# Performance work log

Hardware: AMD Instinct MI355X
Metric: run time of the kernel (lower is better)

Reference implementation:

```python
import jax, jax.numpy as jnp
import numpy as np

CONFIGS = [(4, 2, 1, 1), (4, 4, 3, 3)]  # (k, stride, pad, dilation) per level


def conv2d(x, w, b, stride=1, pad=1):
    y = jax.lax.conv_general_dilated(x, w, (stride, stride), [(pad, pad), (pad, pad)],
                                     dimension_numbers=('NCHW', 'OIHW', 'NCHW'))
    return y + b[None, :, None, None]


def deform_conv(x, offset, mask, wgt, b, k, stride, pad, dil):
    """Modulated deformable conv v2 (zero padding, bilinear sampling).
    x: [B,Cin,Hin,Win]; offset: [B,2K,H,W] interleaved (dy_i,dx_i); mask: [B,K,H,W]."""
    B, Cin, Hin, Win = x.shape
    _, _, H, W = mask.shape
    K = k * k
    dy = offset[:, 0::2]  # [B,K,H,W]
    dx = offset[:, 1::2]
    ks = jnp.arange(k, dtype=offset.dtype) * dil
    kyf = jnp.repeat(ks, k)  # [K], ky-major to match weight.reshape(Cout,Cin,K)
    kxf = jnp.tile(ks, k)
    oy = jnp.arange(H, dtype=offset.dtype) * stride - pad
    ox = jnp.arange(W, dtype=offset.dtype) * stride - pad
    py = (kyf[:, None] + oy[None, :])[None, :, :, None] + dy  # [B,K,H,W]
    px = (kxf[:, None] + ox[None, :])[None, :, None, :] + dx

    def per_image(img, pyi, pxi, mi):
        imgf = img.reshape(Cin, -1)
        y0 = jnp.floor(pyi)
        x0 = jnp.floor(pxi)
        ly = pyi - y0
        lx = pxi - x0
        y0i = y0.astype(jnp.int32)
        x0i = x0.astype(jnp.int32)

        def corner(yi, xi, wt):
            valid = (yi >= 0) & (yi < Hin) & (xi >= 0) & (xi < Win)
            lin = (jnp.clip(yi, 0, Hin - 1) * Win + jnp.clip(xi, 0, Win - 1)).reshape(-1)
            v = imgf[:, lin].reshape(Cin, K, H, W)
            return v * (wt * valid)[None]

        s = (corner(y0i, x0i, (1 - ly) * (1 - lx))
             + corner(y0i, x0i + 1, (1 - ly) * lx)
             + corner(y0i + 1, x0i, ly * (1 - lx))
             + corner(y0i + 1, x0i + 1, ly * lx))
        return s * mi[None]  # [Cin,K,H,W]

    sampled = jax.vmap(per_image)(x, py, px, mask)  # [B,Cin,K,H,W]
    out = jnp.einsum('bikhw,oik->bohw', sampled, wgt.reshape(wgt.shape[0], Cin, K))
    return out + b[None, :, None, None]


def setup_inputs():
    key = jax.random.key(0)
    ks = jax.random.split(key, 16)
    B, C, H = 4, 256, 40
    K = 16  # k*k with k=4
    dcn_std = 1.0 / np.sqrt(C * K)
    res_std = 1.0 / np.sqrt(C * 9)
    return {
        'f0': jax.random.normal(ks[0], (B, C, H * 4, H * 4), jnp.float32),
        'f1': jax.random.normal(ks[1], (B, C, H * 2, H * 2), jnp.float32),
        'f2': jax.random.normal(ks[2], (B, C, H, H), jnp.float32),
        'com_w0': jax.random.normal(ks[3], (3 * K, C, 3, 3), jnp.float32) * 0.01,
        'com_b0': jax.random.normal(ks[4], (3 * K,), jnp.float32) * 0.01,
        'com_w1': jax.random.normal(ks[5], (3 * K, C, 3, 3), jnp.float32) * 0.01,
        'com_b1': jax.random.normal(ks[6], (3 * K,), jnp.float32) * 0.01,
        'dcn_w0': jax.random.normal(ks[7], (C, C, 4, 4), jnp.float32) * dcn_std,
        'dcn_b0': jnp.zeros((C,), jnp.float32),
        'dcn_w1': jax.random.normal(ks[8], (C, C, 4, 4), jnp.float32) * dcn_std,
        'dcn_b1': jnp.zeros((C,), jnp.float32),
        'res_w': jax.random.normal(ks[9], (C, C, 3, 3), jnp.float32) * res_std,
        'res_b': jnp.zeros((C,), jnp.float32),
    }


def reference(f0, f1, f2, com_w0, com_b0, com_w1, com_b1,
              dcn_w0, dcn_b0, dcn_w1, dcn_b1, res_w, res_b):
    features = [f0, f1, f2]
    com = [(com_w0, com_b0), (com_w1, com_b1)]
    dcn = [(dcn_w0, dcn_b0), (dcn_w1, dcn_b1)]
    repeat, levels = 2, 3
    fh = features[-1]
    f = fh
    for _ in range(repeat):
        for l in range(levels - 1):
            k, s, p, d = CONFIGS[l]
            K = k * k
            om = conv2d(f, com[l][0], com[l][1])
            offset = jnp.concatenate([om[:, :K], om[:, K:2 * K]], axis=1)
            m = jax.nn.sigmoid(om[:, 2 * K:])
            dc = deform_conv(features[levels - 2 - l], offset, m, dcn[l][0], dcn[l][1], k, s, p, d)
            f = jax.nn.relu(dc) + f
    return fh + conv2d(f, res_w, res_b)
```

## Files before the change

### kernel.cpp

```cpp
#include <hip/hip_runtime.h>

#define HW40 1600
typedef unsigned short ushort_t;
typedef __attribute__((ext_vector_type(8))) short short8;
typedef __attribute__((ext_vector_type(4))) short short4v;
typedef __attribute__((ext_vector_type(4))) float f4v;

__device__ __forceinline__ float bu(ushort_t u) {
  union { unsigned i; float f; } x; x.i = ((unsigned)u) << 16; return x.f;
}
__device__ __forceinline__ ushort_t fb(float f) {
  union { float f; unsigned i; } x; x.f = f;
  unsigned r = x.i + 0x7FFFu + ((x.i >> 16) & 1u);
  return (ushort_t)(r >> 16);
}

#define GLD16(g, l)                                                            \
  __builtin_amdgcn_global_load_lds(                                            \
      (const __attribute__((address_space(1))) void*)(g),                      \
      (__attribute__((address_space(3))) void*)(l), 16, 0, 0)

#define PART_STRIDE 1638400

__global__ __launch_bounds__(256) void prep_all(
    const float* __restrict__ com_w0, const float* __restrict__ com_w1,
    const float* __restrict__ res_w, const float* __restrict__ dcn_w0,
    const float* __restrict__ dcn_w1, ushort_t* __restrict__ Acom0,
    ushort_t* __restrict__ Acom1, ushort_t* __restrict__ Ares,
    ushort_t* __restrict__ A0, ushort_t* __restrict__ A1,
    ushort_t* __restrict__ zp) {
  __shared__ float s[4096];
  const int g = blockIdx.x;
  const int t = threadIdx.x;
  if (g < 3456) {
    const float* src; ushort_t* dst; int Cout_src; int base;
    if (g < 576)       { src = com_w0; dst = Acom0; Cout_src = 48;  base = g; }
    else if (g < 1152) { src = com_w1; dst = Acom1; Cout_src = 48;  base = g - 576; }
    else               { src = res_w;  dst = Ares;  Cout_src = 256; base = g - 1152; }
    const int idx = base * 256 + t;
    const int co = idx / 2304;
    const int k  = idx - co * 2304;
    const int cin = k & 255, tap = k >> 8;
    dst[idx] = (co < Cout_src) ? fb(src[(size_t)co * 2304 + cin * 9 + tap]) : (ushort_t)0;
  } else if (g < 3968) {
    const int lg = g - 3456;
    const int co = lg & 255;
    const float* w = (lg < 256) ? dcn_w0 : dcn_w1;
    ushort_t* A = (lg < 256) ? A0 : A1;
    const float4* wp = (const float4*)(w + (size_t)co * 4096);
#pragma unroll
    for (int q = 0; q < 4; ++q) ((float4*)s)[t + q * 256] = wp[t + q * 256];
    __syncthreads();
    const int i = t >> 4, cb = (t & 15) * 16;
    ushort_t tmp[16];
#pragma unroll
    for (int j = 0; j < 16; ++j) tmp[j] = fb(s[(cb + j) * 16 + i]);
    ushort_t* op = A + (size_t)co * 4096 + t * 16;
    ((uint4*)op)[0] = ((uint4*)tmp)[0];
    ((uint4*)op)[1] = ((uint4*)tmp)[1];
  } else {
    zp[t] = 0;
  }
}

__global__ __launch_bounds__(256) void nhwc_all(const float* __restrict__ f2,
                                                const float* __restrict__ f1,
                                                const float* __restrict__ f0,
                                                ushort_t* __restrict__ ft40,
                                                ushort_t* __restrict__ f1t,
                                                ushort_t* __restrict__ f0t) {
  __shared__ __align__(16) ushort_t tile[32][264];
  const int gx = blockIdx.x;
  const float* x; ushort_t* xt; int HW, sblk;
  if (gx < 50)       { x = f2; xt = ft40; HW = 1600;  sblk = gx; }
  else if (gx < 250) { x = f1; xt = f1t;  HW = 6400;  sblk = gx - 50; }
  else               { x = f0; xt = f0t;  HW = 25600; sblk = gx - 250; }
  const int s0 = sblk * 32, b = blockIdx.z;
  const int t = threadIdx.x;
  const int sp4 = (t & 7) * 4;
  const int cbase = (t >> 3) * 4;
  const float* xb = x + (size_t)b * 256 * HW + s0 + sp4;
#pragma unroll
  for (int q = 0; q < 2; ++q) {
    const int cc = cbase + q * 128;
    const float4 v0 = *(const float4*)(xb + (size_t)(cc + 0) * HW);
    const float4 v1 = *(const float4*)(xb + (size_t)(cc + 1) * HW);
    const float4 v2 = *(const float4*)(xb + (size_t)(cc + 2) * HW);
    const float4 v3 = *(const float4*)(xb + (size_t)(cc + 3) * HW);
    ushort_t p0[4] = {fb(v0.x), fb(v1.x), fb(v2.x), fb(v3.x)};
    ushort_t p1[4] = {fb(v0.y), fb(v1.y), fb(v2.y), fb(v3.y)};
    ushort_t p2[4] = {fb(v0.z), fb(v1.z), fb(v2.z), fb(v3.z)};
    ushort_t p3[4] = {fb(v0.w), fb(v1.w), fb(v2.w), fb(v3.w)};
    *(short4v*)(&tile[sp4 + 0][cc]) = *(short4v*)p0;
    *(short4v*)(&tile[sp4 + 1][cc]) = *(short4v*)p1;
    *(short4v*)(&tile[sp4 + 2][cc]) = *(short4v*)p2;
    *(short4v*)(&tile[sp4 + 3][cc]) = *(short4v*)p3;
  }
  __syncthreads();
  const int c8 = (t & 31) * 8;
  const int spb = t >> 5;
  ushort_t* ob = xt + ((size_t)b * HW + s0) * 256;
#pragma unroll
  for (int q2 = 0; q2 < 4; ++q2) {
    const int sp = spb + q2 * 8;
    short8 v = *(const short8*)(&tile[sp][c8]);
    *(short8*)(ob + (size_t)sp * 256 + c8) = v;
  }
}

__global__ __launch_bounds__(256) void sample_kernel(
    const ushort_t* __restrict__ xt, const ushort_t* __restrict__ part,
    const float* __restrict__ cbias, ushort_t* __restrict__ colT,
    int Hin, int Win, int stride, int pad, int dil) {
  __shared__ int4  gL[128];
  __shared__ float4 gW[128];
  const int g = blockIdx.x;
  const int work = (g & 7) * 100 + (g >> 3);
  const int b = work / 200;
  const int px0 = (work - b * 200) * 8;
  const int t = threadIdx.x;
  const int HWin = Hin * Win;

  if (t < 128) {
    const int px_l = t & 7, i = t >> 3;
    const int p = px0 + px_l;
    const int n = b * 1600 + p;
    const int ph = p / 40, pw = p - (p / 40) * 40;
    float dy = cbias[2 * i], dx = cbias[2 * i + 1], mzr = cbias[32 + i];
#pragma unroll
    for (int kz = 0; kz < 8; ++kz) {
      const ushort_t* pp = part + (size_t)kz * PART_STRIDE + n;
      dy  += bu(pp[(size_t)(2 * i) * 6400]);
      dx  += bu(pp[(size_t)(2 * i + 1) * 6400]);
      mzr += bu(pp[(size_t)(32 + i) * 6400]);
    }
    float mz = 1.f / (1.f + expf(-mzr));
    float py = (float)(ph * stride - pad + (i >> 2) * dil) + dy;
    float px = (float)(pw * stride - pad + (i & 3) * dil) + dx;
    float y0f = floorf(py), x0f = floorf(px);
    float ly = py - y0f, lx = px - x0f;
    int y0 = (int)y0f, x0 = (int)x0f;
    int y1 = y0 + 1, x1 = x0 + 1;
    float hy = 1.f - ly, hx = 1.f - lx;
    float w00 = hy * hx * mz, w01 = hy * lx * mz;
    float w10 = ly * hx * mz, w11 = ly * lx * mz;
    if (y0 < 0 || y0 >= Hin) { w00 = 0.f; w01 = 0.f; }
    if (y1 < 0 || y1 >= Hin) { w10 = 0.f; w11 = 0.f; }
    if (x0 < 0 || x0 >= Win) { w00 = 0.f; w10 = 0.f; }
    if (x1 < 0 || x1 >= Win) { w01 = 0.f; w11 = 0.f; }
    int cy0 = min(max(y0, 0), Hin - 1), cy1 = min(max(y1, 0), Hin - 1);
    int cx0 = min(max(x0, 0), Win - 1), cx1 = min(max(x1, 0), Win - 1);
    gL[t] = make_int4((cy0 * Win + cx0) * 256, (cy0 * Win + cx1) * 256,
                      (cy1 * Win + cx0) * 256, (cy1 * Win + cx1) * 256);
    gW[t] = make_float4(w00, w01, w10, w11);
  }
  __syncthreads();

  const ushort_t* xtb = xt + (size_t)b * HWin * 256;
  const int wv = t >> 6, l = t & 63;
  const int half = l >> 5;
  const int cin8 = (l & 31) * 8;

#pragma unroll 2
  for (int it = 0; it < 16; ++it) {
    const int pr = it * 8 + wv * 2 + half;
    const int4 G = gL[pr];
    const float4 W = gW[pr];
    short8 c00 = *(const short8*)(xtb + G.x + cin8);
    short8 c01 = *(const short8*)(xtb + G.y + cin8);
    short8 c10 = *(const short8*)(xtb + G.z + cin8);
    short8 c11 = *(const short8*)(xtb + G.w + cin8);
    short8 rr;
#pragma unroll
    for (int j = 0; j < 8; ++j) {
      float v = W.x * bu((ushort_t)c00[j]) + W.y * bu((ushort_t)c01[j]) +
                W.z * bu((ushort_t)c10[j]) + W.w * bu((ushort_t)c11[j]);
      rr[j] = (short)fb(v);
    }
    const int px_l = pr & 7, i = pr >> 3;
    *(short8*)(colT + ((size_t)(b * 1600 + px0 + px_l) * 4096 + i * 256 + cin8)) = rr;
  }
}

__global__ __launch_bounds__(256) void gemm_deform(const ushort_t* __restrict__ A,
                                                   const ushort_t* __restrict__ B,
                                                   ushort_t* __restrict__ part) {
  __shared__ ushort_t sA[128 * 32];
  __shared__ ushort_t sB[128 * 32];
  const int g = blockIdx.x;
  const int kz = g & 3, mt = (g >> 2) & 1, nt = g >> 3;
  const int t = threadIdx.x;
  const int wv = t >> 6, l = t & 63;
  const int wm = wv >> 1, wn = wv & 1;

  f4v acc[4][4];
#pragma unroll
  for (int a = 0; a < 4; ++a)
#pragma unroll
    for (int bb = 0; bb < 4; ++bb) acc[a][bb] = (f4v)(0.f);

  const int ra = t >> 2;
  const int q  = ((t & 3) - (ra >> 1)) & 3;
  const size_t aoff = (size_t)(mt * 128 + ra) * 4096 + q * 8;
  const size_t boff = (size_t)(nt * 128 + ra) * 4096 + q * 8;
  ushort_t* lA = sA + t * 8;
  ushort_t* lB = sB + t * 8;

  int k0 = kz * 1024;
  const int lm = l & 15;
  const int koff = (((l >> 4) + (lm >> 1)) & 3) * 8;

  for (int step = 0; step < 32; ++step, k0 += 32) {
    __syncthreads();
    GLD16(A + aoff + k0, lA);
    GLD16(A + aoff + (size_t)64 * 4096 + k0, lA + 2048);
    GLD16(B + boff + k0, lB);
    GLD16(B + boff + (size_t)64 * 4096 + k0, lB + 2048);
    __syncthreads();
    short8 af[4], bfr[4];
#pragma unroll
    for (int fm = 0; fm < 4; ++fm)
      af[fm] = *(const short8*)(sA + (wm * 64 + fm * 16 + lm) * 32 + koff);
#pragma unroll
    for (int fn = 0; fn < 4; ++fn)
      bfr[fn] = *(const short8*)(sB + (wn * 64 + fn * 16 + lm) * 32 + koff);
#pragma unroll
    for (int fm = 0; fm < 4; ++fm)
#pragma unroll
      for (int fn = 0; fn < 4; ++fn)
        acc[fm][fn] = __builtin_amdgcn_mfma_f32_16x16x32_bf16(af[fm], bfr[fn],
                                                              acc[fm][fn], 0, 0, 0);
  }

  const int row_l = (l >> 4) * 4;
  ushort_t* pb = part + (size_t)kz * PART_STRIDE;
#pragma unroll
  for (int fm = 0; fm < 4; ++fm) {
#pragma unroll
    for (int fn = 0; fn < 4; ++fn) {
      const int n = nt * 128 + wn * 64 + fn * 16 + lm;
#pragma unroll
      for (int r = 0; r < 4; ++r) {
        const int m = mt * 128 + wm * 64 + fm * 16 + row_l + r;
        pb[(size_t)m * 6400 + n] = fb(acc[fm][fn][r]);
      }
    }
  }
}

template <int MTILE, int KZ>
__global__ __launch_bounds__(256) void gemm_conv3(const ushort_t* __restrict__ A,
                                                  const ushort_t* __restrict__ ft,
                                                  const ushort_t* __restrict__ zp,
                                                  ushort_t* __restrict__ part,
                                                  int ksteps) {
  constexpr int FN = (MTILE == 128) ? 4 : 2;
  __shared__ ushort_t sA[MTILE * 32];
  __shared__ ushort_t sB[128 * 32];
  const int g = blockIdx.x;
  const int kz = g % KZ;
  const int r = g / KZ;
  const int mt = (MTILE == 128) ? (r & 1) : 0;
  const int nt = (MTILE == 128) ? (r >> 1) : r;
  const int t = threadIdx.x;
  const int wv = t >> 6, l = t & 63;
  const int wm = (MTILE == 128) ? (wv >> 1) : 0;
  const int wn = (MTILE == 128) ? (wv & 1) : wv;

  f4v acc[4][FN];
#pragma unroll
  for (int a = 0; a < 4; ++a)
#pragma unroll
    for (int bb = 0; bb < FN; ++bb) acc[a][bb] = (f4v)(0.f);

  const int ra = t >> 2;
  const int q  = ((t & 3) - (ra >> 1)) & 3;
  const int qc = q * 8;
  const size_t aoff = (size_t)(mt * MTILE + ra) * 2304 + qc;
  const int n0 = nt * 128 + ra;
  const int n1 = n0 + 64;
  const int b0 = n0 / 1600, p0 = n0 - b0 * 1600;
  const int b1 = n1 / 1600, p1 = n1 - b1 * 1600;
  const int ph0 = p0 / 40, pw0 = p0 - (p0 / 40) * 40;
  const int ph1 = p1 / 40, pw1 = p1 - (p1 / 40) * 40;
  const ushort_t* fp0 = ft + (size_t)n0 * 256 + qc;
  const ushort_t* fp1 = ft + (size_t)n1 * 256 + qc;
  ushort_t* lA = sA + t * 8;
  ushort_t* lB = sB + t * 8;

  int k0 = kz * ksteps * 32;
  const int lm = l & 15;
  const int koff = (((l >> 4) + (lm >> 1)) & 3) * 8;

  for (int step = 0; step < ksteps; ++step, k0 += 32) {
    const int tap = k0 >> 8, c0 = k0 & 255;
    const int ky = tap / 3;
    const int dy = ky - 1, dx = (tap - ky * 3) - 1;
    const int off = (dy * 40 + dx) * 256 + c0;
    const bool ok0 = ((unsigned)(ph0 + dy) < 40u) & ((unsigned)(pw0 + dx) < 40u);
    const bool ok1 = ((unsigned)(ph1 + dy) < 40u) & ((unsigned)(pw1 + dx) < 40u);
    const ushort_t* s0 = ok0 ? (fp0 + off) : zp;
    const ushort_t* s1 = ok1 ? (fp1 + off) : zp;
    __syncthreads();
    GLD16(A + aoff + k0, lA);
    if (MTILE == 128) GLD16(A + aoff + (size_t)64 * 2304 + k0, lA + 2048);
    GLD16(s0, lB);
    GLD16(s1, lB + 2048);
    __syncthreads();
    short8 af[4], bfr[FN];
#pragma unroll
    for (int fm = 0; fm < 4; ++fm)
      af[fm] = *(const short8*)(sA + (wm * 64 + fm * 16 + lm) * 32 + koff);
#pragma unroll
    for (int fn = 0; fn < FN; ++fn)
      bfr[fn] = *(const short8*)(sB + (wn * (16 * FN) + fn * 16 + lm) * 32 + koff);
#pragma unroll
    for (int fm = 0; fm < 4; ++fm)
#pragma unroll
      for (int fn = 0; fn < FN; ++fn)
        acc[fm][fn] = __builtin_amdgcn_mfma_f32_16x16x32_bf16(af[fm], bfr[fn],
                                                              acc[fm][fn], 0, 0, 0);
  }

  const int row_l = (l >> 4) * 4;
  ushort_t* pb = part + (size_t)kz * PART_STRIDE;
#pragma unroll
  for (int fm = 0; fm < 4; ++fm) {
#pragma unroll
    for (int fn = 0; fn < FN; ++fn) {
      const int n = nt * 128 + wn * (16 * FN) + fn * 16 + lm;
#pragma unroll
      for (int r = 0; r < 4; ++r) {
        const int m = mt * MTILE + wm * 64 + fm * 16 + row_l + r;
        pb[(size_t)m * 6400 + n] = fb(acc[fm][fn][r]);
      }
    }
  }
}

template <int NKZ>
__global__ __launch_bounds__(256) void epi_fused(const ushort_t* __restrict__ part,
                                                 const float* __restrict__ bias,
                                                 const float* __restrict__ src,
                                                 float* __restrict__ dst,
                                                 ushort_t* __restrict__ ft, int relu) {
  __shared__ __align__(16) ushort_t tile[32][72];
  const int t = threadIdx.x;
  const int p0 = blockIdx.x * 64, c0 = blockIdx.y * 32, b = blockIdx.z;
  const int co_l = t >> 3, pg = t & 7;
  const int co = c0 + co_l;
  const size_t n = (size_t)b * 1600 + p0 + pg * 8;

  float a[8] = {0.f, 0.f, 0.f, 0.f, 0.f, 0.f, 0.f, 0.f};
#pragma unroll
  for (int kz = 0; kz < NKZ; ++kz) {
    short8 pp = *(const short8*)(part + (size_t)kz * PART_STRIDE + (size_t)co * 6400 + n);
#pragma unroll
    for (int j = 0; j < 8; ++j) a[j] += bu((ushort_t)pp[j]);
  }
  const float bv = bias[co];
  const size_t fo = ((size_t)b * 256 + co) * 1600 + p0 + pg * 8;
  float4 s0 = *(const float4*)(src + fo);
  float4 s1 = *(const float4*)(src + fo + 4);
  const float sv[8] = {s0.x, s0.y, s0.z, s0.w, s1.x, s1.y, s1.z, s1.w};
  float o[8];
#pragma unroll
  for (int j = 0; j < 8; ++j) {
    float v = a[j] + bv;
    if (relu) v = fmaxf(v, 0.f);
    o[j] = v + sv[j];
  }
  float4 o0 = {o[0], o[1], o[2], o[3]};
  float4 o1 = {o[4], o[5], o[6], o[7]};
  *(float4*)(dst + fo) = o0;
  *(float4*)(dst + fo + 4) = o1;

  if (ft) {
    short8 rr;
#pragma unroll
    for (int j = 0; j < 8; ++j) rr[j] = (short)fb(o[j]);
    *(short8*)(&tile[co_l][pg * 8]) = rr;
    __syncthreads();
    const int p_l = t >> 2, cb = (t & 3) * 8;
    short8 v;
#pragma unroll
    for (int j = 0; j < 8; ++j) v[j] = (short)tile[cb + j][p_l];
    *(short8*)(ft + ((size_t)(b * 1600 + p0 + p_l)) * 256 + c0 + cb) = v;
  }
}

extern "C" void kernel_launch(void* const* d_in, const int* in_sizes, int n_in,
                              void* d_out, int out_size, void* d_ws, size_t ws_size,
                              hipStream_t stream) {
  (void)in_sizes; (void)n_in; (void)out_size; (void)ws_size;
  const float* f0     = (const float*)d_in[0];
  const float* f1     = (const float*)d_in[1];
  const float* f2     = (const float*)d_in[2];
  const float* com_w0 = (const float*)d_in[3];
  const float* com_b0 = (const float*)d_in[4];
  const float* com_w1 = (const float*)d_in[5];
  const float* com_b1 = (const float*)d_in[6];
  const float* dcn_w0 = (const float*)d_in[7];
  const float* dcn_b0 = (const float*)d_in[8];
  const float* dcn_w1 = (const float*)d_in[9];
  const float* dcn_b1 = (const float*)d_in[10];
  const float* res_w  = (const float*)d_in[11];
  const float* res_b  = (const float*)d_in[12];
  float* out = (float*)d_out;
  float* ws  = (float*)d_ws;

  float*    fbuf  = ws + 0;
  ushort_t* A0    = (ushort_t*)(ws + 1700000);
  ushort_t* A1    = (ushort_t*)(ws + 2230000);
  ushort_t* Acom0 = (ushort_t*)(ws + 2760000);
  ushort_t* Acom1 = (ushort_t*)(ws + 2840000);
  ushort_t* Ares  = (ushort_t*)(ws + 2920000);
  ushort_t* ft40  = (ushort_t*)(ws + 3220000);
  ushort_t* f1t   = (ushort_t*)(ws + 4050000);
  ushort_t* f0t   = (ushort_t*)(ws + 7330000);
  ushort_t* colT  = (ushort_t*)(ws + 20440000);
  ushort_t* part  = (ushort_t*)(ws + 33550000);
  ushort_t* zp    = (ushort_t*)(ws + 40110000);

  prep_all<<<3969, 256, 0, stream>>>(com_w0, com_w1, res_w, dcn_w0, dcn_w1,
                                     Acom0, Acom1, Ares, A0, A1, zp);
  nhwc_all<<<dim3(1050, 1, 4), 256, 0, stream>>>(f2, f1, f0, ft40, f1t, f0t);

  const float* fsrc = f2;
  for (int s = 0; s < 4; ++s) {
    int l = s & 1;
    gemm_conv3<64, 8><<<400, 256, 0, stream>>>(l ? Acom1 : Acom0, ft40, zp, part, 9);
    if (l == 0) {
      sample_kernel<<<800, 256, 0, stream>>>(f1t, part, com_b0, colT, 80, 80, 2, 1, 1);
    } else {
      sample_kernel<<<800, 256, 0, stream>>>(f0t, part, com_b1, colT, 160, 160, 4, 3, 3);
    }
    gemm_deform<<<400, 256, 0, stream>>>(l ? A1 : A0, colT, part);
    epi_fused<4><<<dim3(25, 8, 4), 256, 0, stream>>>(part, l ? dcn_b1 : dcn_b0, fsrc,
                                                     fbuf, ft40, 1);
    fsrc = fbuf;
  }
  gemm_conv3<128, 8><<<800, 256, 0, stream>>>(Ares, ft40, zp, part, 9);
  epi_fused<8><<<dim3(25, 8, 4), 256, 0, stream>>>(part, res_b, f2, out, nullptr, 0);
}
```

Measured before the change: 539.6 us.

## Enlarge NHWC transpose tiles and swizzle GEMM block mapping across XCDs

Rewrites the NCHW-to-NHWC bf16 conversion kernel to process 128 (or 64) spatial positions per block with wider coalesced row reads and a flat 1D grid. It also remaps block indices in the deform and conv3 GEMMs so neighbouring tiles are grouped by XCD, improving L2 reuse of shared A/B panels. The larger LDS tile may reduce occupancy of the transpose kernel.

```diff
diff --git a/kernel.cpp b/kernel.cpp
--- a/kernel.cpp
+++ b/kernel.cpp
@@ -63,48 +63,62 @@
   }
 }
 
+template <int SPT>
+__device__ __forceinline__ void nhwc_body(const float* __restrict__ x,
+                                          ushort_t* __restrict__ xt,
+                                          int HW, int s0, int b,
+                                          ushort_t (*tile)[264]) {
+  const int t = threadIdx.x;
+  const int l = t & 63, wv = t >> 6;
+  constexpr int LPC = SPT / 4;
+  constexpr int CPW = (64 / LPC) * 4;
+  constexpr int NIT = 256 / (4 * CPW);
+  const int spl = (l & (LPC - 1)) * 4;
+  const int cgrp = (l / LPC) * 4;
+  const float* xb = x + (size_t)b * 256 * HW + s0 + spl;
+#pragma unroll
+  for (int it = 0; it < NIT; ++it) {
+    const int cb = (it * 4 + wv) * CPW + cgrp;
+    const float4 v0 = *(const float4*)(xb + (size_t)(cb + 0) * HW);
+    const float4 v1 = *(const float4*)(xb + (size_t)(cb + 1) * HW);
+    const float4 v2 = *(const float4*)(xb + (size_t)(cb + 2) * HW);
+    const float4 v3 = *(const float4*)(xb + (size_t)(cb + 3) * HW);
+    ushort_t p0[4] = {fb(v0.x), fb(v1.x), fb(v2.x), fb(v3.x)};
+    ushort_t p1[4] = {fb(v0.y), fb(v1.y), fb(v2.y), fb(v3.y)};
+    ushort_t p2[4] = {fb(v0.z), fb(v1.z), fb(v2.z), fb(v3.z)};
+    ushort_t p3[4] = {fb(v0.w), fb(v1.w), fb(v2.w), fb(v3.w)};
+    *(short4v*)(&tile[spl + 0][cb]) = *(short4v*)p0;
+    *(short4v*)(&tile[spl + 1][cb]) = *(short4v*)p1;
+    *(short4v*)(&tile[spl + 2][cb]) = *(short4v*)p2;
+    *(short4v*)(&tile[spl + 3][cb]) = *(short4v*)p3;
+  }
+  __syncthreads();
+  const int c8 = (t & 31) * 8;
+  const int spb = t >> 5;
+  ushort_t* ob = xt + ((size_t)b * HW + s0) * 256;
+#pragma unroll
+  for (int q = 0; q < SPT / 8; ++q) {
+    const int sp = spb + q * 8;
+    *(short8*)(ob + (size_t)sp * 256 + c8) = *(const short8*)(&tile[sp][c8]);
+  }
+}
+
 __global__ __launch_bounds__(256) void nhwc_all(const float* __restrict__ f2,
                                                 const float* __restrict__ f1,
                                                 const float* __restrict__ f0,
                                                 ushort_t* __restrict__ ft40,
                                                 ushort_t* __restrict__ f1t,
                                                 ushort_t* __restrict__ f0t) {
-  __shared__ __align__(16) ushort_t tile[32][264];
+  __shared__ __align__(16) ushort_t tile[128][264];
   const int gx = blockIdx.x;
-  const float* x; ushort_t* xt; int HW, sblk;
-  if (gx < 50)       { x = f2; xt = ft40; HW = 1600;  sblk = gx; }
-  else if (gx < 250) { x = f1; xt = f1t;  HW = 6400;  sblk = gx - 50; }
-  else               { x = f0; xt = f0t;  HW = 25600; sblk = gx - 250; }
-  const int s0 = sblk * 32, b = blockIdx.z;
-  const int t = threadIdx.x;
-  const int sp4 = (t & 7) * 4;
-  const int cbase = (t >> 3) * 4;
-  const float* xb = x + (size_t)b * 256 * HW + s0 + sp4;
-#pragma unroll
-  for (int q = 0; q < 2; ++q) {
-    const int cc = cbase + q * 128;
-    const float4 v0 = *(const float4*)(xb + (size_t)(cc + 0) * HW);
-    const float4 v1 = *(const float4*)(xb + (size_t)(cc + 1) * HW);
-    const float4 v2 = *(const float4*)(xb + (size_t)(cc + 2) * HW);
-    const float4 v3 = *(const float4*)(xb + (size_t)(cc + 3) * HW);
-    ushort_t p0[4] = {fb(v0.x), fb(v1.x), fb(v2.x), fb(v3.x)};
-    ushort_t p1[4] = {fb(v0.y), fb(v1.y), fb(v2.y), fb(v3.y)};
-    ushort_t p2[4] = {fb(v0.z), fb(v1.z), fb(v2.z), fb(v3.z)};
-    ushort_t p3[4] = {fb(v0.w), fb(v1.w), fb(v2.w), fb(v3.w)};
-    *(short4v*)(&tile[sp4 + 0][cc]) = *(short4v*)p0;
-    *(short4v*)(&tile[sp4 + 1][cc]) = *(short4v*)p1;
-    *(short4v*)(&tile[sp4 + 2][cc]) = *(short4v*)p2;
-    *(short4v*)(&tile[sp4 + 3][cc]) = *(short4v*)p3;
-  }
-  __syncthreads();
-  const int c8 = (t & 31) * 8;
-  const int spb = t >> 5;
-  ushort_t* ob = xt + ((size_t)b * HW + s0) * 256;
-#pragma unroll
-  for (int q2 = 0; q2 < 4; ++q2) {
-    const int sp = spb + q2 * 8;
-    short8 v = *(const short8*)(&tile[sp][c8]);
-    *(short8*)(ob + (size_t)sp * 256 + c8) = v;
+  if (gx < 800) {
+    nhwc_body<128>(f0, f0t, 25600, (gx % 200) * 128, gx / 200, tile);
+  } else if (gx < 1000) {
+    const int g1 = gx - 800;
+    nhwc_body<128>(f1, f1t, 6400, (g1 % 50) * 128, g1 / 50, tile);
+  } else {
+    const int g2 = gx - 1000;
+    nhwc_body<64>(f2, ft40, 1600, (g2 % 25) * 64, g2 / 25, tile);
   }
 }
 
@@ -188,7 +202,8 @@
   __shared__ ushort_t sA[128 * 32];
   __shared__ ushort_t sB[128 * 32];
   const int g = blockIdx.x;
-  const int kz = g & 3, mt = (g >> 2) & 1, nt = g >> 3;
+  const int id = (g & 7) * 50 + (g >> 3);
+  const int mt = id & 1, kz = (id >> 1) & 3, nt = id >> 3;
   const int t = threadIdx.x;
   const int wv = t >> 6, l = t & 63;
   const int wm = wv >> 1, wn = wv & 1;
@@ -258,8 +273,9 @@
   __shared__ ushort_t sA[MTILE * 32];
   __shared__ ushort_t sB[128 * 32];
   const int g = blockIdx.x;
-  const int kz = g % KZ;
-  const int r = g / KZ;
+  const int id = (g & 7) * (gridDim.x >> 3) + (g >> 3);
+  const int kz = id % KZ;
+  const int r = id / KZ;
   const int mt = (MTILE == 128) ? (r & 1) : 0;
   const int nt = (MTILE == 128) ? (r >> 1) : r;
   const int t = threadIdx.x;
@@ -424,7 +440,7 @@
 
   prep_all<<<3969, 256, 0, stream>>>(com_w0, com_w1, res_w, dcn_w0, dcn_w1,
                                      Acom0, Acom1, Ares, A0, A1, zp);
-  nhwc_all<<<dim3(1050, 1, 4), 256, 0, stream>>>(f2, f1, f0, ft40, f1t, f0t);
+  nhwc_all<<<dim3(1100, 1, 1), 256, 0, stream>>>(f2, f1, f0, ft40, f1t, f0t);
 
   const float* fsrc = f2;
   for (int s = 0; s < 4; ++s) {
```

Result: faster. 517.4 us (-4.1%).
